# Optimization experiments

Hardware: AMD Instinct MI355X
Metric: run time of the kernel (lower is better)

The kernel has to match this reference:

```python
import jax, jax.numpy as jnp
import numpy as np

EPS = 1e-5
LAMB = 1.0
N_VARS = 40000
N_EDGES = 200000
N_CONF = 100000
FEAT = 128
DOM = 4
T_MAX = 3


def setup_inputs() -> dict:
    key = jax.random.key(0)
    ks = jax.random.split(key, 16)
    # initial node states: torch.rand then row-normalized (F.normalize dim=1)
    s = jax.random.uniform(ks[0], (N_VARS, FEAT), dtype=jnp.float32)
    state0 = s / jnp.maximum(jnp.linalg.norm(s, axis=1, keepdims=True), 1e-12)
    def lin(k, fan_in, shape):
        return jax.random.normal(k, shape, dtype=jnp.float32) / np.sqrt(fan_in)
    inp = {
        'state0': state0,
        'W1': lin(ks[1], 2 * FEAT, (2 * FEAT, FEAT)),
        'b1': jnp.zeros((FEAT,), jnp.float32),
        'W2': lin(ks[2], FEAT, (FEAT, FEAT)),
        'b2': jnp.zeros((FEAT,), jnp.float32),
        'ln_g': jnp.ones((FEAT,), jnp.float32),
        'ln_b': jnp.zeros((FEAT,), jnp.float32),
        'bn_g': jnp.ones((FEAT,), jnp.float32),
        'bn_b': jnp.zeros((FEAT,), jnp.float32),
        'Wd': lin(ks[3], FEAT, (FEAT, DOM)),
        'bd': jnp.zeros((DOM,), jnp.float32),
        # positive relation/confidence matrices so -log(...) is finite
        'relation': jax.random.uniform(ks[4], (DOM, DOM), jnp.float32, 0.1, 1.0),
        'confidence_mat': jax.random.uniform(ks[5], (DOM, DOM), jnp.float32, 0.1, 1.0),
        # positive degrees (divisor)
        'degrees': jax.random.uniform(ks[6], (N_VARS,), jnp.float32, 1.0, 33.0),
        'idx_left': jax.random.randint(ks[7], (N_EDGES,), 0, N_VARS, jnp.int32),
        'idx_right': jax.random.randint(ks[8], (N_EDGES,), 0, N_VARS, jnp.int32),
        'idx_left_pos': jax.random.randint(ks[9], (N_CONF,), 0, N_VARS, jnp.int32),
        'idx_right_pos': jax.random.randint(ks[10], (N_CONF,), 0, N_VARS, jnp.int32),
        'iterations': T_MAX,
    }
    return inp


def reference(state0, W1, b1, W2, b2, ln_g, ln_b, bn_g, bn_b, Wd, bd,
              relation, confidence_mat, degrees,
              idx_left, idx_right, idx_left_pos, idx_right_pos, iterations):
    N, F = state0.shape
    E = idx_left.shape[0]
    degs = degrees[:, None]

    def mlp(x):  # Linear-ReLU-Linear-ReLU-LayerNorm
        h = jax.nn.relu(x @ W1 + b1)
        h = jax.nn.relu(h @ W2 + b2)
        mu = jnp.mean(h, axis=-1, keepdims=True)
        var = jnp.var(h, axis=-1, keepdims=True)  # biased, like torch LayerNorm
        return ln_g * (h - mu) * jax.lax.rsqrt(var + EPS) + ln_b

    state = state0
    logits_list = []
    for _ in range(iterations):
        xl = state[idx_left]          # [E, F] gather
        xr = state[idx_right]
        # mpnn(in_right=xl, in_left=xr): in_lr = cat(xr, xl); in_rl = cat(xl, xr)
        msg = jnp.concatenate([jnp.concatenate([xr, xl], axis=1),
                               jnp.concatenate([xl, xr], axis=1)], axis=0)  # [2E, 2F]
        h = mlp(msg)
        agg = (jnp.zeros((N, F), state.dtype)
               .at[idx_left].add(h[:E])
               .at[idx_right].add(h[E:]))  # scatter-add messages
        rec = agg / degs
        # BatchNorm1d, training mode (batch stats over nodes)
        mu = jnp.mean(rec, axis=0)
        var = jnp.var(rec, axis=0)
        state = bn_g * (rec - mu) * jax.lax.rsqrt(var + EPS) + bn_b
        logits_list.append(state @ Wd + bd)

    phi = jax.nn.softmax(jnp.stack(logits_list, axis=1), axis=2)  # [N, T, D]
    T, D = phi.shape[1], phi.shape[2]
    all_phi = phi.reshape(N, T * D)

    def pair_loss(mat, il, ir, denom):
        pl = all_phi[il].reshape(-1, D)   # [E*T, D]
        pr = all_phi[ir].reshape(-1, D)
        s = jnp.sum((pl @ mat) * pr, axis=1)
        return jnp.sum(-jnp.log(s)) / denom

    n_conflicts = jnp.float32(E)
    n_confidence = jnp.float32(idx_left_pos.shape[0])
    loss = (pair_loss(relation, idx_left, idx_right, n_conflicts)
            + LAMB * pair_loss(confidence_mat, idx_left_pos, idx_right_pos, 10.0 * n_confidence))

    assignment = jnp.argmax(phi, axis=2).astype(jnp.int32)  # [N, T]
    valid = relation[assignment[idx_left], assignment[idx_right]]  # [E, T]
    edge_conflicts = 1.0 - valid
    n_conf = jnp.sum(edge_conflicts[:, -1])
    conflict_ratio = n_conf / n_conflicts
    return (loss, conflict_ratio, phi, edge_conflicts, assignment[:, -1], n_conf)
```

## Files before the change

### kernel.cpp

```cpp
#include <hip/hip_runtime.h>
#include <math.h>

#define N_VARS 40000
#define FEAT 128
#define N_EDGES 200000
#define N_MSG (2*N_EDGES)
#define N_CONFP 100000
#define T_ITERS 3
#define EPSF 1e-5f

#define NB_CONF 782
#define NB_PAIR 1172
#define NB_STAT 157
#define NB_STAT2 625
#define NB_MSG64 6250
#define OUT_TOTAL 1120003
#define NCONF_SLOT 1120002

typedef short short8 __attribute__((ext_vector_type(8)));
typedef float floatx4 __attribute__((ext_vector_type(4)));
typedef unsigned short ushort4v __attribute__((ext_vector_type(4)));
typedef unsigned uint4v __attribute__((ext_vector_type(4)));

__device__ __forceinline__ float scrub0(float x){
  unsigned u = __float_as_uint(x);
  return ((u & 0x7F800000u) == 0x7F800000u) ? 0.f : x;
}
__device__ __forceinline__ unsigned short f2bf_rne(float x){
  unsigned u = __float_as_uint(x);
  u += 0x7FFFu + ((u >> 16) & 1u);
  return (unsigned short)(u >> 16);
}
__device__ __forceinline__ float bf2f(unsigned short h){
  return __uint_as_float(((unsigned)h) << 16);
}
__device__ __forceinline__ unsigned cvtpk(float lo, float hi){
  unsigned r;
  asm("v_cvt_pk_bf16_f32 %0, %1, %2" : "=v"(r) : "v"(lo), "v"(hi));
  return r;
}

__global__ __launch_bounds__(256) void k_zero_int(int* __restrict__ p, int n){
  int i = blockIdx.x*256 + threadIdx.x;
  if (i < n) p[i] = 0;
}

__global__ __launch_bounds__(256) void k_hist(const int* __restrict__ idxL,
    const int* __restrict__ idxR, int* __restrict__ cnt){
  int m = blockIdx.x*256 + threadIdx.x;
  if (m < N_MSG){
    int t = (m < N_EDGES) ? idxL[m] : idxR[m - N_EDGES];
    atomicAdd(&cnt[t], 1);
  }
}
__global__ __launch_bounds__(256) void k_scan1(const int* __restrict__ cnt,
    int* __restrict__ pos, int* __restrict__ blk_tot){
  const int tid = threadIdx.x;
  const int idx = blockIdx.x*256 + tid;
  int v = (idx < N_VARS) ? cnt[idx] : 0;
  __shared__ int sh[256];
  sh[tid] = v;
  __syncthreads();
#pragma unroll
  for (int o = 1; o < 256; o <<= 1){
    int add = (tid >= o) ? sh[tid - o] : 0;
    __syncthreads();
    sh[tid] += add;
    __syncthreads();
  }
  if (idx < N_VARS) pos[idx] = sh[tid] - v;
  if (tid == 255) blk_tot[blockIdx.x] = sh[255];
}
__global__ __launch_bounds__(256) void k_scan2(const int* __restrict__ blk_tot,
    int* __restrict__ blk_off){
  const int tid = threadIdx.x;
  int v = (tid < NB_STAT) ? blk_tot[tid] : 0;
  __shared__ int sh[256];
  sh[tid] = v;
  __syncthreads();
#pragma unroll
  for (int o = 1; o < 256; o <<= 1){
    int add = (tid >= o) ? sh[tid - o] : 0;
    __syncthreads();
    sh[tid] += add;
    __syncthreads();
  }
  if (tid < NB_STAT) blk_off[tid] = sh[tid] - v;
}
__global__ __launch_bounds__(256) void k_scan3(int* __restrict__ pos,
    const int* __restrict__ blk_off){
  const int idx = blockIdx.x*256 + threadIdx.x;
  if (idx < N_VARS) pos[idx] += blk_off[blockIdx.x];
}
__global__ __launch_bounds__(256) void k_fill(const int* __restrict__ idxL,
    const int* __restrict__ idxR, int* __restrict__ pos,
    int2* __restrict__ pairs){
  int m = blockIdx.x*256 + threadIdx.x;
  if (m < N_MSG){
    int e = (m < N_EDGES) ? m : (m - N_EDGES);
    int l = idxL[e], r = idxR[e];
    int t = (m < N_EDGES) ? l : r;
    int o = (m < N_EDGES) ? r : l;
    int slot = atomicAdd(&pos[t], 1);
    pairs[slot] = make_int2(t, o);
  }
}

__global__ __launch_bounds__(256) void k_prep2(const float* __restrict__ W2,
                                               const float* __restrict__ W1,
                                               unsigned short* __restrict__ W2pack,
                                               unsigned short* __restrict__ W1pack){
  if (blockIdx.x < 8){
    int gid = blockIdx.x*256 + threadIdx.x;
    int lane = gid & 63;
    int ks = (gid >> 6) & 3;
    int ntg = gid >> 8;
    int kbase = ks*32 + (lane >> 4)*8;
    int n = ntg*16 + (lane & 15);
#pragma unroll
    for (int j = 0; j < 8; ++j)
      W2pack[gid*8 + j] = f2bf_rne(W2[(kbase + j)*FEAT + n]);
  } else {
    int gid = (blockIdx.x - 8)*256 + threadIdx.x;
    int lane = gid & 63;
    int ks = (gid >> 6) & 3;
    int ntg = gid >> 8;
    int kbase = ks*32 + (lane >> 4)*8;
    int n = ntg*16 + (lane & 15);
#pragma unroll
    for (int j = 0; j < 8; ++j){
      int k = kbase + j;
      float v = (n < 128) ? W1[k*FEAT + n] : W1[(128 + k)*FEAT + (n - 128)];
      W1pack[gid*8 + j] = f2bf_rne(v);
    }
  }
}

#define X_STRIDE 136
__global__ __launch_bounds__(256) void k_pq(const float* __restrict__ xf,
                                            const unsigned short* __restrict__ xb,
                                            int src_f32,
                                            const unsigned short* __restrict__ W1pack,
                                            const float* __restrict__ b1v,
                                            unsigned short* __restrict__ PQb,
                                            float* __restrict__ red,
                                            float4* __restrict__ recz){
  __shared__ __align__(16) unsigned short Xbf[32*X_STRIDE];
  const int tid = threadIdx.x;
  const int row0 = blockIdx.x * 32;
  if (blockIdx.x == 0) red[tid] = 0.f;
  {
    const int zid = blockIdx.x*256 + tid;
#pragma unroll
    for (int i = 0; i < 4; ++i)
      recz[zid + i*320000] = make_float4(0.f,0.f,0.f,0.f);
  }
  if (src_f32){
    const int c4 = (tid & 31)*4, g8 = tid >> 5;
#pragma unroll
    for (int r = 0; r < 4; ++r){
      int row = g8*4 + r;
      const float4 v = *(const float4*)&xf[(row0 + row)*FEAT + c4];
      uint2 uu;
      uu.x = cvtpk(v.x, v.y);
      uu.y = cvtpk(v.z, v.w);
      *(uint2*)&Xbf[row*X_STRIDE + c4] = uu;
    }
  } else {
    const int c8 = (tid & 15)*8, g16 = tid >> 4;
#pragma unroll
    for (int r = 0; r < 2; ++r){
      int row = r*16 + g16;
      *(short8*)&Xbf[row*X_STRIDE + c8] = *(const short8*)&xb[(row0 + row)*FEAT + c8];
    }
  }
  __syncthreads();
  const int w = tid >> 6, lane = tid & 63;
  const int quad = lane >> 4, mcol = lane & 15;
  float bi0 = 0.f, bi1 = 0.f, bi2 = 0.f, bi3 = 0.f;
  if (w >= 2){
    int nb = (w - 2)*64 + mcol;
    bi0 = b1v[nb]; bi1 = b1v[nb + 16]; bi2 = b1v[nb + 32]; bi3 = b1v[nb + 48];
  }
#pragma unroll
  for (int mt = 0; mt < 2; ++mt){
    floatx4 a0 = {bi0,bi0,bi0,bi0};
    floatx4 a1 = {bi1,bi1,bi1,bi1};
    floatx4 a2 = {bi2,bi2,bi2,bi2};
    floatx4 a3 = {bi3,bi3,bi3,bi3};
#pragma unroll
    for (int ks = 0; ks < 4; ++ks){
      short8 a = *(const short8*)&Xbf[(mt*16 + mcol)*X_STRIDE + ks*32 + quad*8];
      const unsigned short* bp = W1pack + ((w*16 + ks)*64 + lane)*8;
      short8 b0 = *(const short8*)(bp);
      short8 b1 = *(const short8*)(bp + 2048);
      short8 b2 = *(const short8*)(bp + 4096);
      short8 b3 = *(const short8*)(bp + 6144);
      a0 = __builtin_amdgcn_mfma_f32_16x16x32_bf16(a, b0, a0, 0, 0, 0);
      a1 = __builtin_amdgcn_mfma_f32_16x16x32_bf16(a, b1, a1, 0, 0, 0);
      a2 = __builtin_amdgcn_mfma_f32_16x16x32_bf16(a, b2, a2, 0, 0, 0);
      a3 = __builtin_amdgcn_mfma_f32_16x16x32_bf16(a, b3, a3, 0, 0, 0);
    }
#pragma unroll
    for (int reg = 0; reg < 4; ++reg){
      unsigned u01 = cvtpk(a0[reg], a1[reg]);
      unsigned u23 = cvtpk(a2[reg], a3[reg]);
      size_t base = (size_t)(row0 + mt*16 + quad*4 + reg)*(2*FEAT) + w*64 + mcol;
      PQb[base]      = (unsigned short)u01;
      PQb[base + 16] = (unsigned short)(u01 >> 16);
      PQb[base + 32] = (unsigned short)u23;
      PQb[base + 48] = (unsigned short)(u23 >> 16);
    }
  }
}

#define U_STRIDE 136
#define ZT_STRIDE 68

__global__ __launch_bounds__(256) void k_msgagg(const unsigned short* __restrict__ PQb,
    const unsigned short* __restrict__ W2pack,
    const float* __restrict__ b2v, const float* __restrict__ ln_g, const float* __restrict__ ln_b,
    const int2* __restrict__ pairs, const float* __restrict__ degrees,
    float* __restrict__ rec){
  __shared__ __align__(16) unsigned short PZ[64*U_STRIDE];
  __shared__ __align__(16) unsigned short Qlds[64*U_STRIDE];
  __shared__ int sTrun[64];
  __shared__ int sTa[64];
  __shared__ float sDinv[64];
  __shared__ int sE[2];
  const int tid = threadIdx.x;
  const int s0 = blockIdx.x * 64;
  const int w = tid >> 6, lane = tid & 63;
  const int ta = pairs[s0 + lane].x;
  const int tn = __shfl_down(ta, 1);
  const bool brk = (lane == 63) ? true : (tn != ta);
  const unsigned long long bm = __ballot(brk);
  const int nruns = __popcll(bm);
  const bool isstart = (lane == 0) || ((bm >> (lane - 1)) & 1ull);
  const int ridlane = (int)__popcll(bm & ((1ull << lane) - 1ull));
  if (isstart) sTrun[ridlane] = ta;
  if (w == 0){
    sTa[lane] = ta;
    sDinv[lane] = 1.f / degrees[ta];
    if (lane == 62) sE[0] = (s0 == 0) ? -1 : pairs[s0 - 1].x;
    if (lane == 63) sE[1] = (s0 + 64 >= N_MSG) ? -1 : pairs[s0 + 64].x;
  }
  const int c8 = (tid & 15)*8, g16 = tid >> 4;
#pragma unroll
  for (int r = 0; r < 4; ++r){
    int row = r*16 + g16;
    int other = pairs[s0 + row].y;
    *(short8*)&PZ[row*U_STRIDE + c8] =
        *(const short8*)&PQb[(size_t)other*(2*FEAT) + c8];
  }
  asm volatile("s_waitcnt lgkmcnt(0)" ::: "memory");
  {
    const int q4 = lane >> 4;
    const int c8l = (lane & 15)*8;
    for (int k = w*4 + q4; k < nruns; k += 16){
      int tgt = sTrun[k];
      *(short8*)&Qlds[k*U_STRIDE + c8l] =
          *(const short8*)&PQb[(size_t)tgt*(2*FEAT) + FEAT + c8l];
    }
  }
  __syncthreads();
  const int quad = lane >> 4, mcol = lane & 15;
  const int rbase = w*16;
  const int myrow = rbase + mcol;
  const int myrid = (int)__popcll(bm & ((1ull << myrow) - 1ull));
  short8 afr[4];
#pragma unroll
  for (int ks = 0; ks < 4; ++ks){
    short8 pc = *(const short8*)&PZ[myrow*U_STRIDE + ks*32 + quad*8];
    short8 qc = *(const short8*)&Qlds[myrid*U_STRIDE + ks*32 + quad*8];
    uint4v pu = *(const uint4v*)&pc;
    uint4v qu = *(const uint4v*)&qc;
    uint4v ou;
#pragma unroll
    for (int d = 0; d < 4; ++d){
      float plo = __uint_as_float(pu[d] << 16);
      float phi = __uint_as_float(pu[d] & 0xFFFF0000u);
      float qlo = __uint_as_float(qu[d] << 16);
      float qhi = __uint_as_float(qu[d] & 0xFFFF0000u);
      ou[d] = cvtpk(fmaxf(plo + qlo, 0.f), fmaxf(phi + qhi, 0.f));
    }
    afr[ks] = *(const short8*)&ou;
  }
  floatx4 acc[8];
#pragma unroll
  for (int nt = 0; nt < 8; ++nt){
    float b = b2v[nt*16 + mcol];
    acc[nt] = (floatx4){b, b, b, b};
  }
#pragma unroll
  for (int ks = 0; ks < 4; ++ks){
#pragma unroll
    for (int nt = 0; nt < 8; ++nt){
      short8 b = *(const short8*)(W2pack + ((nt*4 + ks)*64 + lane)*8);
      acc[nt] = __builtin_amdgcn_mfma_f32_16x16x32_bf16(afr[ks], b, acc[nt], 0, 0, 0);
    }
  }
  float z[8][4];
#pragma unroll
  for (int nt = 0; nt < 8; ++nt){
#pragma unroll
    for (int reg = 0; reg < 4; ++reg) z[nt][reg] = fmaxf(acc[nt][reg], 0.f);
  }
  float ps[4], pq[4];
#pragma unroll
  for (int reg = 0; reg < 4; ++reg){
    ps[reg] = 0.f; pq[reg] = 0.f;
#pragma unroll
    for (int nt = 0; nt < 8; ++nt){
      ps[reg] += z[nt][reg];
      pq[reg] += z[nt][reg]*z[nt][reg];
    }
  }
#pragma unroll
  for (int o = 1; o < 16; o <<= 1){
#pragma unroll
    for (int reg = 0; reg < 4; ++reg){
      ps[reg] += __shfl_xor(ps[reg], o);
      pq[reg] += __shfl_xor(pq[reg], o);
    }
  }
  float muv[4], rvv[4];
#pragma unroll
  for (int reg = 0; reg < 4; ++reg){
    float mu = ps[reg] * (1.f/FEAT);
    float var = fmaxf(pq[reg] * (1.f/FEAT) - mu*mu, 0.f);
    muv[reg] = mu;
    rvv[reg] = rsqrtf(var + EPSF);
  }
  unsigned w0p[8], w1p[8];
#pragma unroll
  for (int nt = 0; nt < 8; ++nt){
    float lg = ln_g[nt*16 + mcol];
    float lb = ln_b[nt*16 + mcol];
    float o0 = scrub0(lg*(z[nt][0] - muv[0])*rvv[0] + lb);
    float o1 = scrub0(lg*(z[nt][1] - muv[1])*rvv[1] + lb);
    float o2 = scrub0(lg*(z[nt][2] - muv[2])*rvv[2] + lb);
    float o3 = scrub0(lg*(z[nt][3] - muv[3])*rvv[3] + lb);
    w0p[nt] = cvtpk(o0, o1);
    w1p[nt] = cvtpk(o2, o3);
  }
  __syncthreads();
#pragma unroll
  for (int nt = 0; nt < 8; ++nt){
    uint2 u; u.x = w0p[nt]; u.y = w1p[nt];
    *(uint2*)&PZ[(nt*16 + mcol)*ZT_STRIDE + rbase + quad*4] = u;
  }
  __syncthreads();
  {
    const int col = tid & 127, h = tid >> 7;
    const int rbeg = h*32;
    const unsigned bmh = (unsigned)(h ? (bm >> 32) : bm);
    ushort4v rv4[8];
#pragma unroll
    for (int k = 0; k < 8; ++k)
      rv4[k] = *(const ushort4v*)&PZ[col*ZT_STRIDE + rbeg + k*4];
    float accv = 0.f;
    int cur = sTa[rbeg];
    bool part = (rbeg == 0) ? (sE[0] == cur) : (sTa[rbeg-1] == cur);
#pragma unroll
    for (int i = 0; i < 32; ++i){
      accv += bf2f((unsigned short)rv4[i >> 2][i & 3]);
      const bool realbrk = (bmh >> i) & 1u;
      if ((i == 31) | realbrk){
        const int r = rbeg + i;
        bool cont = (i == 31) && ((r == 63) ? (sE[1] == cur) : !realbrk);
        float v = accv * sDinv[r];
        float* dst = &rec[(size_t)cur*FEAT + col];
        if (part | cont) atomicAdd(dst, v);
        else *dst = v;
        accv = 0.f;
        part = false;
        if (i < 31) cur = sTa[r + 1];
      }
    }
  }
}

__global__ __launch_bounds__(256) void k_edge(const unsigned short* __restrict__ PQb,
    const unsigned short* __restrict__ W2pack,
    const float* __restrict__ b2v, const float* __restrict__ ln_g, const float* __restrict__ ln_b,
    const int* __restrict__ idxL, const int* __restrict__ idxR,
    float* __restrict__ agg){
  __shared__ __align__(16) unsigned short Ubf[32*U_STRIDE];
  __shared__ float sS[64], sQ[64];
  __shared__ int sTa[32], sTb[32];
  const int tid = threadIdx.x;
  const int m0 = blockIdx.x * 32;
  if (tid < 32){
    int m = m0 + tid;
    int e = (m < N_EDGES) ? m : (m - N_EDGES);
    int l = idxL[e], r = idxR[e];
    sTa[tid] = (m < N_EDGES) ? l : r;
    sTb[tid] = (m < N_EDGES) ? r : l;
  }
  __syncthreads();
  {
    const int c8 = (tid & 15)*8, g16 = tid >> 4;
#pragma unroll
    for (int r = 0; r < 2; ++r){
      int row = r*16 + g16;
      short8 pb = *(const short8*)&PQb[sTb[row]*(2*FEAT) + c8];
      short8 qb = *(const short8*)&PQb[sTa[row]*(2*FEAT) + FEAT + c8];
      float f[8];
#pragma unroll
      for (int j = 0; j < 8; ++j)
        f[j] = fmaxf(bf2f((unsigned short)pb[j]) + bf2f((unsigned short)qb[j]), 0.f);
      uint4 uu;
      uu.x = cvtpk(f[0], f[1]);
      uu.y = cvtpk(f[2], f[3]);
      uu.z = cvtpk(f[4], f[5]);
      uu.w = cvtpk(f[6], f[7]);
      *(uint4*)&Ubf[row*U_STRIDE + c8] = uu;
    }
  }
  __syncthreads();
  const int w = tid >> 6, lane = tid & 63;
  const int mt = w & 1, nhalf = w >> 1;
  const int quad = lane >> 4, mcol = lane & 15;
  float bb0 = b2v[nhalf*64 + 0*16 + mcol];
  float bb1 = b2v[nhalf*64 + 1*16 + mcol];
  float bb2 = b2v[nhalf*64 + 2*16 + mcol];
  float bb3 = b2v[nhalf*64 + 3*16 + mcol];
  floatx4 acc0 = {bb0,bb0,bb0,bb0};
  floatx4 acc1 = {bb1,bb1,bb1,bb1};
  floatx4 acc2 = {bb2,bb2,bb2,bb2};
  floatx4 acc3 = {bb3,bb3,bb3,bb3};
#pragma unroll
  for (int ks = 0; ks < 4; ++ks){
    short8 a = *(const short8*)&Ubf[(mt*16 + mcol)*U_STRIDE + ks*32 + quad*8];
    const unsigned short* bp = W2pack + ((nhalf*4*256) + ks*64 + lane)*8;
    short8 bq0 = *(const short8*)(bp);
    short8 bq1 = *(const short8*)(bp + 2048);
    short8 bq2 = *(const short8*)(bp + 4096);
    short8 bq3 = *(const short8*)(bp + 6144);
    acc0 = __builtin_amdgcn_mfma_f32_16x16x32_bf16(a, bq0, acc0, 0, 0, 0);
    acc1 = __builtin_amdgcn_mfma_f32_16x16x32_bf16(a, bq1, acc1, 0, 0, 0);
    acc2 = __builtin_amdgcn_mfma_f32_16x16x32_bf16(a, bq2, acc2, 0, 0, 0);
    acc3 = __builtin_amdgcn_mfma_f32_16x16x32_bf16(a, bq3, acc3, 0, 0, 0);
  }
  float z[4][4];
#pragma unroll
  for (int nt = 0; nt < 4; ++nt){
    floatx4 a4 = (nt == 0) ? acc0 : (nt == 1) ? acc1 : (nt == 2) ? acc2 : acc3;
#pragma unroll
    for (int reg = 0; reg < 4; ++reg) z[nt][reg] = fmaxf(a4[reg], 0.f);
  }
  float ps[4], pq[4];
#pragma unroll
  for (int reg = 0; reg < 4; ++reg){
    ps[reg] = z[0][reg] + z[1][reg] + z[2][reg] + z[3][reg];
    pq[reg] = z[0][reg]*z[0][reg] + z[1][reg]*z[1][reg] + z[2][reg]*z[2][reg] + z[3][reg]*z[3][reg];
  }
#pragma unroll
  for (int o = 1; o < 16; o <<= 1){
#pragma unroll
    for (int reg = 0; reg < 4; ++reg){
      ps[reg] += __shfl_xor(ps[reg], o);
      pq[reg] += __shfl_xor(pq[reg], o);
    }
  }
  if (mcol == 0){
#pragma unroll
    for (int reg = 0; reg < 4; ++reg){
      int row = mt*16 + quad*4 + reg;
      sS[nhalf*32 + row] = ps[reg];
      sQ[nhalf*32 + row] = pq[reg];
    }
  }
  __syncthreads();
  int colv[4]; float lgv[4], lbv[4];
#pragma unroll
  for (int nt = 0; nt < 4; ++nt){
    colv[nt] = nhalf*64 + nt*16 + mcol;
    lgv[nt] = ln_g[colv[nt]];
    lbv[nt] = ln_b[colv[nt]];
  }
#pragma unroll
  for (int reg = 0; reg < 4; ++reg){
    int row = mt*16 + quad*4 + reg;
    float s = sS[row] + sS[32 + row];
    float q = sQ[row] + sQ[32 + row];
    float mu = s * (1.f/FEAT);
    float var = fmaxf(q * (1.f/FEAT) - mu*mu, 0.f);
    float rv = rsqrtf(var + EPSF);
    int a = sTa[row];
#pragma unroll
    for (int nt = 0; nt < 4; ++nt){
      float o = scrub0(lgv[nt]*(z[nt][reg] - mu)*rv + lbv[nt]);
      atomicAdd(&agg[a*FEAT + colv[nt]], o);
    }
  }
}

__global__ __launch_bounds__(256) void k_stats(const float* __restrict__ src,
    const float* __restrict__ degrees, int divide, float* __restrict__ red){
  const int tid = threadIdx.x;
  const int j = tid & 127, half_sel = tid >> 7;
  const int n0 = blockIdx.x * 64;
  float s1 = 0.f, s2 = 0.f;
  for (int i = half_sel; i < 64; i += 2){
    int n = n0 + i;
    float v = src[n*FEAT + j];
    if (divide) v /= degrees[n];
    s1 += v;
    s2 += v*v;
  }
  __shared__ float sh1[256], sh2[256];
  sh1[tid] = s1; sh2[tid] = s2;
  __syncthreads();
  if (half_sel == 0){
    atomicAdd(&red[j],       sh1[tid] + sh1[tid+128]);
    atomicAdd(&red[128 + j], sh2[tid] + sh2[tid+128]);
  }
}

__global__ __launch_bounds__(256) void k_bn(const float* __restrict__ src,
    const float* __restrict__ degrees, int divide, const float* __restrict__ red,
    const float* __restrict__ bn_g, const float* __restrict__ bn_b,
    const float* __restrict__ Wd, const float* __restrict__ bd,
    unsigned short* __restrict__ state_bf, int* __restrict__ asg,
    float* __restrict__ out_phi, float* __restrict__ out_asg, int t){
  const int w = threadIdx.x >> 6, l = threadIdx.x & 63;
  const int n = blockIdx.x*4 + w;
  const float invN = 1.f / (float)N_VARS;
  float mu0 = red[l]*invN,     mu1 = red[l+64]*invN;
  float v0  = fmaxf(red[128+l]*invN    - mu0*mu0, 0.f);
  float v1  = fmaxf(red[128+l+64]*invN - mu1*mu1, 0.f);
  float rv0 = rsqrtf(v0 + EPSF);
  float rv1 = rsqrtf(v1 + EPSF);
  float dinv = divide ? (1.f / degrees[n]) : 1.f;
  float r0 = src[n*FEAT + l]    * dinv;
  float r1 = src[n*FEAT + l+64] * dinv;
  float s0 = scrub0(bn_g[l]   *(r0 - mu0)*rv0 + bn_b[l]);
  float s1 = scrub0(bn_g[l+64]*(r1 - mu1)*rv1 + bn_b[l+64]);
  state_bf[n*FEAT + l]    = f2bf_rne(s0);
  state_bf[n*FEAT + l+64] = f2bf_rne(s1);
  float p[4];
#pragma unroll
  for (int d = 0; d < 4; ++d)
    p[d] = s0*Wd[l*4 + d] + s1*Wd[(l+64)*4 + d];
#pragma unroll
  for (int o = 32; o > 0; o >>= 1){
#pragma unroll
    for (int d = 0; d < 4; ++d) p[d] += __shfl_xor(p[d], o);
  }
  if (l == 0){
    float lg[4];
#pragma unroll
    for (int d = 0; d < 4; ++d) lg[d] = scrub0(p[d] + bd[d]);
    float mx = fmaxf(fmaxf(lg[0],lg[1]), fmaxf(lg[2],lg[3]));
    float ex[4]; float ssum = 0.f;
#pragma unroll
    for (int d = 0; d < 4; ++d){ ex[d] = expf(lg[d] - mx); ssum += ex[d]; }
    float inv = 1.f / ssum;
    int am = 0; float bv = -1.f;
#pragma unroll
    for (int d = 0; d < 4; ++d){
      float pv = scrub0(ex[d]*inv);
      out_phi[n*12 + t*4 + d] = pv;
      if (pv > bv){ bv = pv; am = d; }
    }
    asg[n*3 + t] = am;
    if (t == 2) out_asg[n] = (float)am;
  }
}

__global__ __launch_bounds__(256) void k_lossconf(const float* __restrict__ phi,
    const int* __restrict__ iL, const int* __restrict__ iR,
    const int* __restrict__ iLp, const int* __restrict__ iRp,
    const float* __restrict__ rel, const float* __restrict__ conf,
    const int* __restrict__ asg, float* __restrict__ out_ec,
    float* __restrict__ part_l1, float* __restrict__ part_l2,
    float* __restrict__ part_conf){
  if (blockIdx.x < NB_PAIR){
    const int e = blockIdx.x*256 + threadIdx.x;
    float p1 = 0.f, p2 = 0.f;
    if (e < N_EDGES + N_CONFP){
      const int isrel = (e < N_EDGES);
      const int l = isrel ? iL[e] : iLp[e - N_EDGES];
      const int r = isrel ? iR[e] : iRp[e - N_EDGES];
      const float* M = isrel ? rel : conf;
      const float2* plp = (const float2*)(phi + (size_t)l*12);
      const float2* prp = (const float2*)(phi + (size_t)r*12);
      float L[12], R[12];
#pragma unroll
      for (int k = 0; k < 6; ++k){
        float2 a = plp[k], b = prp[k];
        L[2*k] = a.x; L[2*k+1] = a.y;
        R[2*k] = b.x; R[2*k+1] = b.y;
      }
      float acc = 0.f;
#pragma unroll
      for (int tt = 0; tt < 3; ++tt){
        const float* a = L + tt*4;
        const float* b = R + tt*4;
        float s = 0.f;
#pragma unroll
        for (int j = 0; j < 4; ++j){
          float tj = a[0]*M[0*4+j] + a[1]*M[1*4+j] + a[2]*M[2*4+j] + a[3]*M[3*4+j];
          s += tj*b[j];
        }
        s = scrub0(s); s = fmaxf(s, 1e-35f);
        acc -= __logf(s);
      }
      if (isrel) p1 = acc; else p2 = acc;
    }
    __shared__ float sh1[256], sh2[256];
    sh1[threadIdx.x] = p1; sh2[threadIdx.x] = p2;
    __syncthreads();
    for (int k = 128; k > 0; k >>= 1){
      if (threadIdx.x < k){
        sh1[threadIdx.x] += sh1[threadIdx.x + k];
        sh2[threadIdx.x] += sh2[threadIdx.x + k];
      }
      __syncthreads();
    }
    if (threadIdx.x == 0){
      part_l1[blockIdx.x] = sh1[0];
      part_l2[blockIdx.x] = sh2[0];
    }
  } else {
    const int bid = blockIdx.x - NB_PAIR;
    const int e = bid*256 + threadIdx.x;
    float c2 = 0.f;
    if (e < N_EDGES){
      int l = iL[e], r = iR[e];
#pragma unroll
      for (int tt = 0; tt < 3; ++tt){
        int ai = asg[l*3+tt] & 3, bi = asg[r*3+tt] & 3;
        float c = scrub0(1.f - rel[ai*4 + bi]);
        out_ec[e*3 + tt] = c;
        if (tt == 2) c2 = c;
      }
    }
    __shared__ float sh[256];
    sh[threadIdx.x] = c2;
    __syncthreads();
    for (int k = 128; k > 0; k >>= 1){
      if (threadIdx.x < k) sh[threadIdx.x] += sh[threadIdx.x + k];
      __syncthreads();
    }
    if (threadIdx.x == 0) part_conf[bid] = sh[0];
  }
}

__global__ __launch_bounds__(256) void k_fin(const float* __restrict__ part_conf,
    const float* __restrict__ part_l1, const float* __restrict__ part_l2,
    float* __restrict__ out){
  const int tid = threadIdx.x;
  float a = 0.f, ca = 0.f, b = 0.f, cb = 0.f, c = 0.f;
  for (int i = tid; i < NB_PAIR; i += 256){
    float y = part_l1[i] - ca; float t = a + y; ca = (t - a) - y; a = t;
    float y2 = part_l2[i] - cb; float t2 = b + y2; cb = (t2 - b) - y2; b = t2;
  }
  for (int i = tid; i < NB_CONF; i += 256) c += part_conf[i];
  __shared__ float sh1[256], sh2[256], sh3[256];
  sh1[tid] = a; sh2[tid] = b; sh3[tid] = c;
  __syncthreads();
  for (int k = 128; k > 0; k >>= 1){
    if (tid < k){
      sh1[tid] += sh1[tid + k];
      sh2[tid] += sh2[tid + k];
      sh3[tid] += sh3[tid + k];
    }
    __syncthreads();
  }
  if (tid == 0){
    out[0] = sh1[0]/(float)N_EDGES + sh2[0]/(10.f*(float)N_CONFP);
    float nc = sh3[0];
    out[NCONF_SLOT] = nc;
    out[1] = nc / (float)N_EDGES;
  }
}

extern "C" void kernel_launch(void* const* d_in, const int* in_sizes, int n_in,
                              void* d_out, int out_size, void* d_ws, size_t ws_size,
                              hipStream_t stream){
  const float* state0  = (const float*)d_in[0];
  const float* W1      = (const float*)d_in[1];
  const float* b1v     = (const float*)d_in[2];
  const float* W2      = (const float*)d_in[3];
  const float* b2v     = (const float*)d_in[4];
  const float* ln_g    = (const float*)d_in[5];
  const float* ln_b    = (const float*)d_in[6];
  const float* bn_g    = (const float*)d_in[7];
  const float* bn_b    = (const float*)d_in[8];
  const float* Wd      = (const float*)d_in[9];
  const float* bd      = (const float*)d_in[10];
  const float* rel     = (const float*)d_in[11];
  const float* confm   = (const float*)d_in[12];
  const float* degrees = (const float*)d_in[13];
  const int* idxL = (const int*)d_in[14];
  const int* idxR = (const int*)d_in[15];
  const int* iLp  = (const int*)d_in[16];
  const int* iRp  = (const int*)d_in[17];

  char* ws = (char*)d_ws;
  unsigned short* state_bf = (unsigned short*)(ws);
  unsigned short* PQb  = (unsigned short*)(ws + 10240000);
  float*  recagg    = (float*)(ws + 30720000);
  int*    asg       = (int*)  (ws + 51200000);
  float*  red       = (float*)(ws + 51840768);
  float*  part_l1   = (float*)(ws + 51841792);
  float*  part_l2   = (float*)(ws + 51855860);
  float*  part_conf = (float*)(ws + 51869928);
  unsigned short* W2pack = (unsigned short*)(ws + 51873056);
  unsigned short* W1pack = (unsigned short*)(ws + 51905824);
  int*    pos       = (int*)(ws + 51971360);
  int*    cnt       = (int*)(ws + 52131360);
  int2*   pairs     = (int2*)(ws + 52291360);
  int*    blk_tot   = (int*)(ws + 55491360);
  int*    blk_off   = (int*)(ws + 55492384);
  const int use_csr = (ws_size >= (size_t)55493408) ? 1 : 0;

  float* out     = (float*)d_out;
  float* out_phi = out + 2;
  float* out_ec  = out + 480002;
  float* out_asg = out + 1080002;

  k_prep2<<<24, 256, 0, stream>>>(W2, W1, W2pack, W1pack);

  if (use_csr){
    k_zero_int<<<NB_STAT, 256, 0, stream>>>(cnt, N_VARS);
    k_hist<<<(N_MSG + 255)/256, 256, 0, stream>>>(idxL, idxR, cnt);
    k_scan1<<<NB_STAT, 256, 0, stream>>>(cnt, pos, blk_tot);
    k_scan2<<<1, 256, 0, stream>>>(blk_tot, blk_off);
    k_scan3<<<NB_STAT, 256, 0, stream>>>(pos, blk_off);
    k_fill<<<(N_MSG + 255)/256, 256, 0, stream>>>(idxL, idxR, pos, pairs);
  }

  for (int t = 0; t < T_ITERS; ++t){
    k_pq<<<N_VARS/32, 256, 0, stream>>>(state0, state_bf, (t == 0) ? 1 : 0, W1pack, b1v,
                                        PQb, red, (float4*)recagg);
    if (use_csr){
      k_msgagg<<<NB_MSG64, 256, 0, stream>>>(PQb, W2pack, b2v, ln_g, ln_b,
                                             pairs, degrees, recagg);
      k_stats<<<NB_STAT2, 256, 0, stream>>>(recagg, degrees, 0, red);
      k_bn<<<N_VARS/4, 256, 0, stream>>>(recagg, degrees, 0, red, bn_g, bn_b, Wd, bd,
                                         state_bf, asg, out_phi, out_asg, t);
    } else {
      k_edge<<<N_MSG/32, 256, 0, stream>>>(PQb, W2pack, b2v, ln_g, ln_b, idxL, idxR, recagg);
      k_stats<<<NB_STAT2, 256, 0, stream>>>(recagg, degrees, 1, red);
      k_bn<<<N_VARS/4, 256, 0, stream>>>(recagg, degrees, 1, red, bn_g, bn_b, Wd, bd,
                                         state_bf, asg, out_phi, out_asg, t);
    }
  }
  k_lossconf<<<NB_PAIR + NB_CONF, 256, 0, stream>>>(out_phi, idxL, idxR, iLp, iRp, rel, confm,
                                                    asg, out_ec, part_l1, part_l2, part_conf);
  k_fin<<<1, 256, 0, stream>>>(part_conf, part_l1, part_l2, out);
}
```

Before: 561.1 us.

## Stage PQ output through LDS for coalesced stores; gather P/Q directly in msgagg

```diff
diff --git a/kernel.cpp b/kernel.cpp
--- a/kernel.cpp
+++ b/kernel.cpp
@@ -137,6 +137,7 @@
 }
 
 #define X_STRIDE 136
+#define PQ_OSTRIDE 264
 __global__ __launch_bounds__(256) void k_pq(const float* __restrict__ xf,
                                             const unsigned short* __restrict__ xb,
                                             int src_f32,
@@ -145,7 +146,7 @@
                                             unsigned short* __restrict__ PQb,
                                             float* __restrict__ red,
                                             float4* __restrict__ recz){
-  __shared__ __align__(16) unsigned short Xbf[32*X_STRIDE];
+  __shared__ __align__(16) unsigned short S[32*PQ_OSTRIDE];
   const int tid = threadIdx.x;
   const int row0 = blockIdx.x * 32;
   if (blockIdx.x == 0) red[tid] = 0.f;
@@ -164,14 +165,14 @@
       uint2 uu;
       uu.x = cvtpk(v.x, v.y);
       uu.y = cvtpk(v.z, v.w);
-      *(uint2*)&Xbf[row*X_STRIDE + c4] = uu;
+      *(uint2*)&S[row*X_STRIDE + c4] = uu;
     }
   } else {
     const int c8 = (tid & 15)*8, g16 = tid >> 4;
 #pragma unroll
     for (int r = 0; r < 2; ++r){
       int row = r*16 + g16;
-      *(short8*)&Xbf[row*X_STRIDE + c8] = *(const short8*)&xb[(row0 + row)*FEAT + c8];
+      *(short8*)&S[row*X_STRIDE + c8] = *(const short8*)&xb[(row0 + row)*FEAT + c8];
     }
   }
   __syncthreads();
@@ -182,6 +183,7 @@
     int nb = (w - 2)*64 + mcol;
     bi0 = b1v[nb]; bi1 = b1v[nb + 16]; bi2 = b1v[nb + 32]; bi3 = b1v[nb + 48];
   }
+  floatx4 A[2][4];
 #pragma unroll
   for (int mt = 0; mt < 2; ++mt){
     floatx4 a0 = {bi0,bi0,bi0,bi0};
@@ -190,7 +192,7 @@
     floatx4 a3 = {bi3,bi3,bi3,bi3};
 #pragma unroll
     for (int ks = 0; ks < 4; ++ks){
-      short8 a = *(const short8*)&Xbf[(mt*16 + mcol)*X_STRIDE + ks*32 + quad*8];
+      short8 a = *(const short8*)&S[(mt*16 + mcol)*X_STRIDE + ks*32 + quad*8];
       const unsigned short* bp = W1pack + ((w*16 + ks)*64 + lane)*8;
       short8 b0 = *(const short8*)(bp);
       short8 b1 = *(const short8*)(bp + 2048);
@@ -201,16 +203,30 @@
       a2 = __builtin_amdgcn_mfma_f32_16x16x32_bf16(a, b2, a2, 0, 0, 0);
       a3 = __builtin_amdgcn_mfma_f32_16x16x32_bf16(a, b3, a3, 0, 0, 0);
     }
+    A[mt][0] = a0; A[mt][1] = a1; A[mt][2] = a2; A[mt][3] = a3;
+  }
+  __syncthreads();
+#pragma unroll
+  for (int mt = 0; mt < 2; ++mt){
 #pragma unroll
     for (int reg = 0; reg < 4; ++reg){
-      unsigned u01 = cvtpk(a0[reg], a1[reg]);
-      unsigned u23 = cvtpk(a2[reg], a3[reg]);
-      size_t base = (size_t)(row0 + mt*16 + quad*4 + reg)*(2*FEAT) + w*64 + mcol;
-      PQb[base]      = (unsigned short)u01;
-      PQb[base + 16] = (unsigned short)(u01 >> 16);
-      PQb[base + 32] = (unsigned short)u23;
-      PQb[base + 48] = (unsigned short)(u23 >> 16);
-    }
+      unsigned u01 = cvtpk(A[mt][0][reg], A[mt][1][reg]);
+      unsigned u23 = cvtpk(A[mt][2][reg], A[mt][3][reg]);
+      int row = mt*16 + quad*4 + reg;
+      int cb = w*64 + mcol;
+      S[row*PQ_OSTRIDE + cb]      = (unsigned short)u01;
+      S[row*PQ_OSTRIDE + cb + 16] = (unsigned short)(u01 >> 16);
+      S[row*PQ_OSTRIDE + cb + 32] = (unsigned short)u23;
+      S[row*PQ_OSTRIDE + cb + 48] = (unsigned short)(u23 >> 16);
+    }
+  }
+  __syncthreads();
+  {
+    const int orow = tid >> 3, ocg = (tid & 7)*32;
+    const size_t gbase = (size_t)(row0 + orow)*(2*FEAT) + ocg;
+#pragma unroll
+    for (int j = 0; j < 4; ++j)
+      *(short8*)&PQb[gbase + j*8] = *(const short8*)&S[orow*PQ_OSTRIDE + ocg + j*8];
   }
 }
 
@@ -222,9 +238,7 @@
     const float* __restrict__ b2v, const float* __restrict__ ln_g, const float* __restrict__ ln_b,
     const int2* __restrict__ pairs, const float* __restrict__ degrees,
     float* __restrict__ rec){
-  __shared__ __align__(16) unsigned short PZ[64*U_STRIDE];
-  __shared__ __align__(16) unsigned short Qlds[64*U_STRIDE];
-  __shared__ int sTrun[64];
+  __shared__ __align__(16) unsigned short Ubf[64*U_STRIDE];
   __shared__ int sTa[64];
   __shared__ float sDinv[64];
   __shared__ int sE[2];
@@ -235,57 +249,63 @@
   const int tn = __shfl_down(ta, 1);
   const bool brk = (lane == 63) ? true : (tn != ta);
   const unsigned long long bm = __ballot(brk);
-  const int nruns = __popcll(bm);
-  const bool isstart = (lane == 0) || ((bm >> (lane - 1)) & 1ull);
-  const int ridlane = (int)__popcll(bm & ((1ull << lane) - 1ull));
-  if (isstart) sTrun[ridlane] = ta;
   if (w == 0){
     sTa[lane] = ta;
     sDinv[lane] = 1.f / degrees[ta];
     if (lane == 62) sE[0] = (s0 == 0) ? -1 : pairs[s0 - 1].x;
     if (lane == 63) sE[1] = (s0 + 64 >= N_MSG) ? -1 : pairs[s0 + 64].x;
   }
-  const int c8 = (tid & 15)*8, g16 = tid >> 4;
-#pragma unroll
-  for (int r = 0; r < 4; ++r){
-    int row = r*16 + g16;
-    int other = pairs[s0 + row].y;
-    *(short8*)&PZ[row*U_STRIDE + c8] =
-        *(const short8*)&PQb[(size_t)other*(2*FEAT) + c8];
-  }
-  asm volatile("s_waitcnt lgkmcnt(0)" ::: "memory");
   {
-    const int q4 = lane >> 4;
-    const int c8l = (lane & 15)*8;
-    for (int k = w*4 + q4; k < nruns; k += 16){
-      int tgt = sTrun[k];
-      *(short8*)&Qlds[k*U_STRIDE + c8l] =
-          *(const short8*)&PQb[(size_t)tgt*(2*FEAT) + FEAT + c8l];
+    const int c8 = (tid & 15)*8, g16 = tid >> 4;
+    int2 pr4[4];
+#pragma unroll
+    for (int r = 0; r < 4; ++r) pr4[r] = pairs[s0 + r*16 + g16];
+    short8 pb[4], qb[4];
+#pragma unroll
+    for (int r = 0; r < 4; ++r){
+      pb[r] = *(const short8*)&PQb[(size_t)pr4[r].y*(2*FEAT) + c8];
+      qb[r] = *(const short8*)&PQb[(size_t)pr4[r].x*(2*FEAT) + FEAT + c8];
+    }
+#pragma unroll
+    for (int r = 0; r < 4; ++r){
+      int row = r*16 + g16;
+      uint4v pu = *(const uint4v*)&pb[r];
+      uint4v qu = *(const uint4v*)&qb[r];
+      uint4 uu;
+      {
+        float plo = __uint_as_float(pu[0] << 16);
+        float phi = __uint_as_float(pu[0] & 0xFFFF0000u);
+        float qlo = __uint_as_float(qu[0] << 16);
+        float qhi = __uint_as_float(qu[0] & 0xFFFF0000u);
+        uu.x = cvtpk(fmaxf(plo + qlo, 0.f), fmaxf(phi + qhi, 0.f));
+      }
+      {
+        float plo = __uint_as_float(pu[1] << 16);
+        float phi = __uint_as_float(pu[1] & 0xFFFF0000u);
+        float qlo = __uint_as_float(qu[1] << 16);
+        float qhi = __uint_as_float(qu[1] & 0xFFFF0000u);
+        uu.y = cvtpk(fmaxf(plo + qlo, 0.f), fmaxf(phi + qhi, 0.f));
+      }
+      {
+        float plo = __uint_as_float(pu[2] << 16);
+        float phi = __uint_as_float(pu[2] & 0xFFFF0000u);
+        float qlo = __uint_as_float(qu[2] << 16);
+        float qhi = __uint_as_float(qu[2] & 0xFFFF0000u);
+        uu.z = cvtpk(fmaxf(plo + qlo, 0.f), fmaxf(phi + qhi, 0.f));
+      }
+      {
+        float plo = __uint_as_float(pu[3] << 16);
+        float phi = __uint_as_float(pu[3] & 0xFFFF0000u);
+        float qlo = __uint_as_float(qu[3] << 16);
+        float qhi = __uint_as_float(qu[3] & 0xFFFF0000u);
+        uu.w = cvtpk(fmaxf(plo + qlo, 0.f), fmaxf(phi + qhi, 0.f));
+      }
+      *(uint4*)&Ubf[row*U_STRIDE + c8] = uu;
     }
   }
   __syncthreads();
   const int quad = lane >> 4, mcol = lane & 15;
   const int rbase = w*16;
-  const int myrow = rbase + mcol;
-  const int myrid = (int)__popcll(bm & ((1ull << myrow) - 1ull));
-  short8 afr[4];
-#pragma unroll
-  for (int ks = 0; ks < 4; ++ks){
-    short8 pc = *(const short8*)&PZ[myrow*U_STRIDE + ks*32 + quad*8];
-    short8 qc = *(const short8*)&Qlds[myrid*U_STRIDE + ks*32 + quad*8];
-    uint4v pu = *(const uint4v*)&pc;
-    uint4v qu = *(const uint4v*)&qc;
-    uint4v ou;
-#pragma unroll
-    for (int d = 0; d < 4; ++d){
-      float plo = __uint_as_float(pu[d] << 16);
-      float phi = __uint_as_float(pu[d] & 0xFFFF0000u);
-      float qlo = __uint_as_float(qu[d] << 16);
-      float qhi = __uint_as_float(qu[d] & 0xFFFF0000u);
-      ou[d] = cvtpk(fmaxf(plo + qlo, 0.f), fmaxf(phi + qhi, 0.f));
-    }
-    afr[ks] = *(const short8*)&ou;
-  }
   floatx4 acc[8];
 #pragma unroll
   for (int nt = 0; nt < 8; ++nt){
@@ -294,10 +314,11 @@
   }
 #pragma unroll
   for (int ks = 0; ks < 4; ++ks){
+    short8 a = *(const short8*)&Ubf[(rbase + mcol)*U_STRIDE + ks*32 + quad*8];
 #pragma unroll
     for (int nt = 0; nt < 8; ++nt){
       short8 b = *(const short8*)(W2pack + ((nt*4 + ks)*64 + lane)*8);
-      acc[nt] = __builtin_amdgcn_mfma_f32_16x16x32_bf16(afr[ks], b, acc[nt], 0, 0, 0);
+      acc[nt] = __builtin_amdgcn_mfma_f32_16x16x32_bf16(a, b, acc[nt], 0, 0, 0);
     }
   }
   float z[8][4];
@@ -348,7 +369,7 @@
 #pragma unroll
   for (int nt = 0; nt < 8; ++nt){
     uint2 u; u.x = w0p[nt]; u.y = w1p[nt];
-    *(uint2*)&PZ[(nt*16 + mcol)*ZT_STRIDE + rbase + quad*4] = u;
+    *(uint2*)&Ubf[(nt*16 + mcol)*ZT_STRIDE + rbase + quad*4] = u;
   }
   __syncthreads();
   {
@@ -358,7 +379,7 @@
     ushort4v rv4[8];
 #pragma unroll
     for (int k = 0; k < 8; ++k)
-      rv4[k] = *(const ushort4v*)&PZ[col*ZT_STRIDE + rbeg + k*4];
+      rv4[k] = *(const ushort4v*)&Ubf[col*ZT_STRIDE + rbeg + k*4];
     float accv = 0.f;
     int cur = sTa[rbeg];
     bool part = (rbeg == 0) ? (sE[0] == cur) : (sTa[rbeg-1] == cur);
```

Measured after the change: 548.6 us. 1.02x faster.
